# Performance work log

Measured on AMD Instinct MI355X. Metric: run time of the kernel, lower is better.

The kernel has to match this reference:

```python
import jax, jax.numpy as jnp
import numpy as np

B, T = 64, 256
CHAR_V, CHAR_D = 8000, 128
WORD_V, WORD_D = 100000, 300
POS_V, POS_D = 30, 64
SPO_D = 20
D = CHAR_D + WORD_D + POS_D + SPO_D  # 512
L, H, KD, VD, INNER = 4, 8, 64, 64, 2048
C = 25  # num tag classes


def _layer_norm(x, g, b, eps=1e-5):
    m = jnp.mean(x, axis=-1, keepdims=True)
    v = jnp.mean(jnp.square(x - m), axis=-1, keepdims=True)
    return (x - m) * jax.lax.rsqrt(v + eps) * g + b


def setup_inputs() -> dict:
    key = jax.random.key(0)
    ks = jax.random.split(key, 40)
    s = 0.05
    n = lambda k, shp, sc=0.05: jax.random.normal(k, shp, jnp.float32) * sc
    return {
        "char": jax.random.randint(ks[0], (B, T), 0, CHAR_V),
        "word": jax.random.randint(ks[1], (B, T), 0, WORD_V),
        "pos": jax.random.randint(ks[2], (B, T), 0, POS_V),
        "spo": jax.random.normal(ks[3], (B, SPO_D), jnp.float32),
        "seq_len": jax.random.randint(ks[4], (B,), 1, T + 1),
        "tag": jax.random.randint(ks[5], (B, T), 0, C),
        "char_table": n(ks[6], (CHAR_V, CHAR_D)),
        "word_table": n(ks[7], (WORD_V, WORD_D)),
        "pos_table": n(ks[8], (POS_V, POS_D)),
        "ln0_g": jnp.ones((D,), jnp.float32),
        "ln0_b": jnp.zeros((D,), jnp.float32),
        "Wq": n(ks[9], (L, D, H * KD)), "bq": jnp.zeros((L, H * KD), jnp.float32),
        "Wk": n(ks[10], (L, D, H * KD)), "bk": jnp.zeros((L, H * KD), jnp.float32),
        "Wv": n(ks[11], (L, D, H * VD)), "bv": jnp.zeros((L, H * VD), jnp.float32),
        "Wo": n(ks[12], (L, H * VD, D)), "bo": jnp.zeros((L, D), jnp.float32),
        "ln1_g": jnp.ones((L, D), jnp.float32), "ln1_b": jnp.zeros((L, D), jnp.float32),
        "W1": n(ks[13], (L, D, INNER)), "b1": jnp.zeros((L, INNER), jnp.float32),
        "W2": n(ks[14], (L, INNER, D)), "b2": jnp.zeros((L, D), jnp.float32),
        "ln2_g": jnp.ones((L, D), jnp.float32), "ln2_b": jnp.zeros((L, D), jnp.float32),
        "Wout": n(ks[15], (D, C)), "bout": jnp.zeros((C,), jnp.float32),
        "trans": n(ks[16], (C, C)),
    }


def _forward(spo, char_table, word_table, pos_table, ln0_g, ln0_b,
             Wq, bq, Wk, bk, Wv, bv, Wo, bo, ln1_g, ln1_b,
             W1, b1, W2, b2, ln2_g, ln2_b, Wout, bout, trans,
             char, word, pos, seq_len, tag):
    # mask[b,t] = t < seq_len[b]
    mask = (jnp.arange(T)[None, :] < seq_len[:, None]).astype(jnp.float32)  # [B,T]

    # embed + concat + layernorm (dropout in eval mode = identity)
    x = jnp.concatenate([
        char_table[char], word_table[word], pos_table[pos],
        jnp.broadcast_to(spo[:, None, :], (B, T, SPO_D)),
    ], axis=-1)  # [B,T,D]
    x = _layer_norm(x, ln0_g, ln0_b)

    neg_inf = jnp.finfo(x.dtype).min
    key_ok = mask[:, None, None, :] > 0  # [B,1,1,T] key padding mask
    scale = jnp.sqrt(jnp.asarray(KD, x.dtype))
    for l in range(L):
        q = (x @ Wq[l] + bq[l]).reshape(B, T, H, KD).transpose(0, 2, 1, 3)
        k = (x @ Wk[l] + bk[l]).reshape(B, T, H, KD).transpose(0, 2, 1, 3)
        v = (x @ Wv[l] + bv[l]).reshape(B, T, H, VD).transpose(0, 2, 1, 3)
        scores = jnp.einsum('bhqd,bhkd->bhqk', q, k) / scale
        scores = jnp.where(key_ok, scores, neg_inf)
        attn = jax.nn.softmax(scores, axis=-1)
        ctx = jnp.einsum('bhqk,bhkd->bhqd', attn, v).transpose(0, 2, 1, 3).reshape(B, T, H * VD)
        att_out = ctx @ Wo[l] + bo[l]
        h1 = _layer_norm(att_out + x, ln1_g[l], ln1_b[l])
        ff = jax.nn.relu(h1 @ W1[l] + b1[l]) @ W2[l] + b2[l]
        x = _layer_norm(ff + h1, ln2_g[l], ln2_b[l]) * mask[:, :, None]

    logits = x @ Wout + bout  # [B,T,C]

    # ---- CRF negative log likelihood (include_start_end_trans=False) ----
    lg = logits.transpose(1, 0, 2)  # [T,B,C]
    m = mask.T                      # [T,B]

    def step(alpha, inp):
        emit, mt = inp  # emit [B,C], mt [B]
        tmp = alpha[:, :, None] + trans[None, :, :] + emit[:, None, :]  # [B,C,C]
        new = jax.nn.logsumexp(tmp, axis=1)
        alpha = jnp.where(mt[:, None] > 0, new, alpha)
        return alpha, None

    alpha, _ = jax.lax.scan(step, lg[0], (lg[1:], m[1:]))
    log_z = jax.nn.logsumexp(alpha, axis=-1)  # [B]

    tags_t = tag.T  # [T,B]
    emit_gold = jnp.take_along_axis(lg, tags_t[:, :, None], axis=-1)[..., 0] * m  # [T,B]
    trans_gold = trans[tags_t[:-1], tags_t[1:]] * m[1:]  # [T-1,B]
    gold = emit_gold.sum(0) + trans_gold.sum(0)  # [B]

    return jnp.mean(log_z - gold)


def reference(char, word, pos, spo, seq_len, tag, char_table, word_table, pos_table,
              ln0_g, ln0_b, Wq, bq, Wk, bk, Wv, bv, Wo, bo, ln1_g, ln1_b,
              W1, b1, W2, b2, ln2_g, ln2_b, Wout, bout, trans):
    return _forward(spo, char_table, word_table, pos_table, ln0_g, ln0_b,
                    Wq, bq, Wk, bk, Wv, bv, Wo, bo, ln1_g, ln1_b,
                    W1, b1, W2, b2, ln2_g, ln2_b, Wout, bout, trans,
                    char, word, pos, seq_len, tag)
```

## Files before the change

kernel.cpp:

```cpp
#include <hip/hip_runtime.h>
#include <cmath>

namespace {

constexpr int LT = 4;
constexpr int BB = 64;
constexpr int TT = 256;
constexpr int DD = 512;
constexpr int HH = 8;
constexpr int DH = 64;
constexpr int FF = 2048;
constexpr int CC = 25;
constexpr int M_ALL = BB * TT;
constexpr size_t MB = 1024 * 1024;

typedef __attribute__((ext_vector_type(8))) short short8;
typedef __attribute__((ext_vector_type(4))) short short4_;
typedef __attribute__((ext_vector_type(4))) float f32x4;
typedef __attribute__((ext_vector_type(4))) _Float16 half4;

__device__ __forceinline__ float b2f(unsigned short u) {
  union { unsigned int i; float f; } x; x.i = ((unsigned int)u) << 16; return x.f;
}
__device__ __forceinline__ unsigned short f2b(float f) {
  union { float f; unsigned int i; } x; x.f = f;
  unsigned int r = x.i + 0x7FFFu + ((x.i >> 16) & 1u);
  return (unsigned short)(r >> 16);
}
__device__ __forceinline__ float rdlane(float v, int l) {
  union { float f; unsigned int i; } x; x.f = v;
  x.i = (unsigned int)__builtin_amdgcn_readlane((int)x.i, l);
  return x.f;
}
__device__ __forceinline__ void gl_lds16(const void* g, void* l) {
  __builtin_amdgcn_global_load_lds(
      (const __attribute__((address_space(1))) unsigned int*)g,
      (__attribute__((address_space(3))) unsigned int*)l, 16, 0, 0);
}
__device__ __forceinline__ float wredsum(float v) {
#pragma unroll
  for (int o = 32; o > 0; o >>= 1) v += __shfl_xor(v, o, 64);
  return v;
}

__global__ __launch_bounds__(64) void prefix_k(const int* __restrict__ sl,
                                               int* __restrict__ boff) {
  const int l = threadIdx.x;
  int s = sl[l];
#pragma unroll
  for (int o = 1; o < 64; o <<= 1) {
    const int u = __shfl_up(s, o, 64);
    if (l >= o) s += u;
  }
  boff[l + 1] = s;
  if (l == 0) boff[0] = 0;
}

__global__ __launch_bounds__(256) void rowmap_k(const int* __restrict__ sl,
                                                const int* __restrict__ boff,
                                                int* __restrict__ rowmap) {
  const int b = blockIdx.x, t = threadIdx.x;
  if (t < sl[b]) rowmap[boff[b] + t] = (b << 8) | t;
}

template <int NSRC>
__global__ __launch_bounds__(256) void wconv_k(const float* __restrict__ in0,
                                               const float* __restrict__ in1,
                                               const float* __restrict__ in2,
                                               unsigned short* __restrict__ out,
                                               int K, int N, size_t lstride,
                                               size_t sstride) {
  __shared__ float ts[64][65];
  const int k0 = blockIdx.x * 64, n0 = blockIdx.y * 64;
  const float* in = in0;
  if constexpr (NSRC == 3) {
    const int s = blockIdx.z / LT;
    in = (s == 0) ? in0 : (s == 1 ? in1 : in2);
    in += (size_t)(blockIdx.z % LT) * K * N;
    out += (size_t)(blockIdx.z % LT) * lstride + (size_t)(blockIdx.z / LT) * sstride;
  } else {
    in += (size_t)blockIdx.z * K * N;
    out += (size_t)blockIdx.z * lstride;
  }
  const int tid = threadIdx.x;
  for (int i = tid; i < 1024; i += 256) {
    const int r = i >> 4, c4 = i & 15;
    const float4 f = *(const float4*)&in[(size_t)(k0 + r) * N + n0 + c4 * 4];
    ts[r][c4 * 4 + 0] = f.x; ts[r][c4 * 4 + 1] = f.y;
    ts[r][c4 * 4 + 2] = f.z; ts[r][c4 * 4 + 3] = f.w;
  }
  __syncthreads();
  const int n_r = tid >> 2, kc = (tid & 3) * 16;
  short8 v0, v1;
#pragma unroll
  for (int j = 0; j < 8; ++j) {
    v0[j] = (short)f2b(ts[kc + j][n_r]);
    v1[j] = (short)f2b(ts[kc + 8 + j][n_r]);
  }
  unsigned short* op = out + (size_t)(n0 + n_r) * K + k0 + kc;
  *(short8*)op = v0;
  *(short8*)(op + 8) = v1;
}

__global__ __launch_bounds__(256) void embed_ln0_k(
    const int* __restrict__ ch, const int* __restrict__ wd, const int* __restrict__ ps,
    const float* __restrict__ spo, const float* __restrict__ ctab,
    const float* __restrict__ wtab, const float* __restrict__ ptab,
    const float* __restrict__ g, const float* __restrict__ be,
    const int* __restrict__ sl, const int* __restrict__ boff,
    unsigned short* __restrict__ xc) {
  const int row = blockIdx.x * 4 + (threadIdx.x >> 6);
  const int b = row >> 8, t = row & 255;
  if (t >= sl[b]) return;
  const int orow = boff[b] + t;
  const int lane = threadIdx.x & 63;
  const int ci = ch[row], wi = wd[row], pi = ps[row];
  float v[8];
#pragma unroll
  for (int j = 0; j < 2; ++j) {
    const int d = j * 256 + lane * 4;
    float4 f;
    if (d < 128)      f = *(const float4*)&ctab[(size_t)ci * 128 + d];
    else if (d < 428) f = *(const float4*)&wtab[(size_t)wi * 300 + (d - 128)];
    else if (d < 492) f = *(const float4*)&ptab[(size_t)pi * 64 + (d - 428)];
    else              f = *(const float4*)&spo[(size_t)b * 20 + (d - 492)];
    v[j * 4 + 0] = f.x; v[j * 4 + 1] = f.y; v[j * 4 + 2] = f.z; v[j * 4 + 3] = f.w;
  }
  float s = 0.f;
#pragma unroll
  for (int i = 0; i < 8; ++i) s += v[i];
  const float mean = wredsum(s) * (1.0f / 512.0f);
  float vs = 0.f;
#pragma unroll
  for (int i = 0; i < 8; ++i) { const float d = v[i] - mean; vs += d * d; }
  const float rstd = rsqrtf(wredsum(vs) * (1.0f / 512.0f) + 1e-5f);
#pragma unroll
  for (int j = 0; j < 2; ++j) {
    const int d = j * 256 + lane * 4;
    const float4 gv = *(const float4*)&g[d];
    const float4 bv = *(const float4*)&be[d];
    short4_ ob;
    ob[0] = (short)f2b((v[j * 4 + 0] - mean) * rstd * gv.x + bv.x);
    ob[1] = (short)f2b((v[j * 4 + 1] - mean) * rstd * gv.y + bv.y);
    ob[2] = (short)f2b((v[j * 4 + 2] - mean) * rstd * gv.z + bv.z);
    ob[3] = (short)f2b((v[j * 4 + 3] - mean) * rstd * gv.w + bv.w);
    *(short4_*)&xc[(size_t)orow * DD + d] = ob;
  }
}

template <int EPI, int TM>
__global__ __launch_bounds__(256) void gemm_mfma(
    const unsigned short* __restrict__ A, const unsigned short* __restrict__ Bt,
    const float* __restrict__ bias, const float* __restrict__ bias2,
    const float* __restrict__ bias3, const unsigned short* __restrict__ res,
    const int* __restrict__ Mptr, const int* __restrict__ rowmap,
    void* __restrict__ outv, void* __restrict__ out2v, void* __restrict__ out3v,
    int M, int N, int K) {
  constexpr int MI = TM / 32;
  const int Mp = Mptr[0];
  const int m0 = blockIdx.y * TM, n0 = blockIdx.x * 128;
  if (m0 >= Mp) return;
  __shared__ unsigned short As[TM * 64];
  __shared__ unsigned short Bs[128 * 64];
  const int tid = threadIdx.x;
  const int wid = tid >> 6, lane = tid & 63;
  const int wr = wid >> 1, wc = wid & 1;
  const int cl = lane & 15, rg = lane >> 4;
  f32x4 acc[MI][4];
#pragma unroll
  for (int i = 0; i < MI; ++i)
#pragma unroll
    for (int j = 0; j < 4; ++j) acc[i][j] = (f32x4){0.f, 0.f, 0.f, 0.f};

  const int rbase = tid >> 3, sl = tid & 7;
  const int sc = 8 * (sl ^ (rbase & 7));

  for (int k0 = 0; k0 < K; k0 += 64) {
    if (k0) __syncthreads();
#pragma unroll
    for (int i = 0; i < TM / 32; ++i) {
      const int r = i * 32 + rbase;
      gl_lds16(A + (size_t)(m0 + r) * K + k0 + sc, (char*)As + (i * 256 + tid) * 16);
    }
#pragma unroll
    for (int i = 0; i < 4; ++i) {
      const int r = i * 32 + rbase;
      gl_lds16(Bt + (size_t)(n0 + r) * K + k0 + sc, (char*)Bs + (i * 256 + tid) * 16);
    }
    __syncthreads();
#pragma unroll
    for (int ks = 0; ks < 2; ++ks) {
      short8 a[MI], b[4];
      const int kbyte = ks * 64 + rg * 16;
#pragma unroll
      for (int f = 0; f < MI; ++f) {
        const int am = wr * (TM / 2) + f * 16 + cl;
        a[f] = *(const short8*)((const char*)As + am * 128 + (kbyte ^ ((am & 7) << 4)));
      }
#pragma unroll
      for (int f = 0; f < 4; ++f) {
        const int bn = wc * 64 + f * 16 + cl;
        b[f] = *(const short8*)((const char*)Bs + bn * 128 + (kbyte ^ ((bn & 7) << 4)));
      }
#pragma unroll
      for (int mi = 0; mi < MI; ++mi)
#pragma unroll
        for (int ni = 0; ni < 4; ++ni)
          acc[mi][ni] = __builtin_amdgcn_mfma_f32_16x16x32_bf16(a[mi], b[ni],
                                                                acc[mi][ni], 0, 0, 0);
    }
  }

  int rm[MI][4];
  if constexpr (EPI == 5) {
#pragma unroll
    for (int mi = 0; mi < MI; ++mi) {
      const int mb_ = m0 + wr * (TM / 2) + mi * 16 + rg * 4;
#pragma unroll
      for (int i = 0; i < 4; ++i)
        rm[mi][i] = (mb_ + i < Mp) ? rowmap[mb_ + i] : -1;
    }
  }

#pragma unroll
  for (int ni = 0; ni < 4; ++ni) {
    const int n = n0 + wc * 64 + ni * 16 + cl;
    float bv;
    if constexpr (EPI == 5) {
      bv = (n < 512) ? bias[n] : (n < 1024 ? bias2[n - 512] : bias3[n - 1024]);
    } else {
      bv = bias[n];
    }
#pragma unroll
    for (int mi = 0; mi < MI; ++mi) {
      if constexpr (EPI == 5) {
        const int hh = (n >> 6) & 7, d = n & 63;
        if (n < 1024) {
          unsigned short* outp = (unsigned short*)((n < 512) ? outv : out2v);
#pragma unroll
          for (int i = 0; i < 4; ++i) {
            const int rmv = rm[mi][i];
            if (rmv >= 0) {
              const int bb = rmv >> 8, tt = rmv & 255;
              outp[(((size_t)(bb * HH + hh) * TT + tt) << 6) + d] =
                  f2b(acc[mi][ni][i] + bv);
            }
          }
        } else {
          const int rm0 = rm[mi][0];
          if (rm0 >= 0 && rm[mi][3] == rm0 + 3) {
            half4 pk;
#pragma unroll
            for (int i = 0; i < 4; ++i) pk[i] = (_Float16)(acc[mi][ni][i] + bv);
            *(half4*)((_Float16*)out3v +
                      ((((size_t)((rm0 >> 8) * HH + hh) * DH + d) << 8) + (rm0 & 255))) = pk;
          } else {
#pragma unroll
            for (int i = 0; i < 4; ++i) {
              const int rmv = rm[mi][i];
              if (rmv >= 0)
                ((_Float16*)out3v)[(((size_t)((rmv >> 8) * HH + hh) * DH + d) << 8) +
                                   (rmv & 255)] = (_Float16)(acc[mi][ni][i] + bv);
            }
          }
        }
      } else {
#pragma unroll
        for (int i = 0; i < 4; ++i) {
          const int m = m0 + wr * (TM / 2) + mi * 16 + rg * 4 + i;
          const float v = acc[mi][ni][i] + bv;
          if constexpr (EPI == 1) {
            ((unsigned short*)outv)[(size_t)m * N + n] = f2b(fmaxf(v, 0.f));
          } else if constexpr (EPI == 7) {
            ((unsigned short*)outv)[(size_t)m * N + n] =
                f2b(v + b2f(res[(size_t)m * N + n]));
          }
        }
      }
    }
  }
}

__global__ __launch_bounds__(256) void attn_mfma_k(
    const unsigned short* __restrict__ qb, const unsigned short* __restrict__ kbp,
    const _Float16* __restrict__ vtp, const int* __restrict__ seq_len,
    const int* __restrict__ boff, unsigned short* __restrict__ cb) {
  __shared__ unsigned short Ks[256 * 64];
  __shared__ _Float16 Vs[64 * 256];
  __shared__ unsigned short Os[64 * 64];
  const int bh = blockIdx.x;
  const int b = bh >> 3, h = bh & 7;
  const int tid = threadIdx.x;
  const int wid = tid >> 6, lane = tid & 63;
  const int cl = lane & 15, rg = lane >> 4;
  const int len = seq_len[b];
  const int off = boff[b];

  {
    const int r = tid >> 3, sl = tid & 7;
#pragma unroll
    for (int i = 0; i < 8; ++i) {
      if (i * 32 < len) {
        const int row = i * 32 + r;
        gl_lds16(kbp + ((size_t)bh * TT + row) * DH + 8 * (sl ^ (row & 7)),
                 (char*)Ks + (i * 256 + tid) * 16);
      }
    }
#pragma unroll
    for (int i = 0; i < 8; ++i) {
      const int u = i * 256 + tid;
      const int vrow = u >> 5, vsl = u & 31;
      gl_lds16(vtp + ((size_t)bh * DH + vrow) * TT + 8 * (vsl ^ (vrow & 7)),
               (char*)Vs + u * 16);
    }
  }
  __syncthreads();

  for (int qt4 = 0; qt4 < 4; ++qt4) {
    if (qt4 * 64 >= len) break;
    f32x4 o[4];
#pragma unroll
    for (int db = 0; db < 4; ++db) o[db] = (f32x4){0.f, 0.f, 0.f, 0.f};
    {
      const int q0 = qt4 * 64 + wid * 16;
      short8 bqf[2];
      const unsigned short* qp = qb + ((size_t)bh * TT + q0 + cl) * DH + rg * 8;
      bqf[0] = *(const short8*)qp;
      bqf[1] = *(const short8*)(qp + 32);
      f32x4 s[16];
#pragma unroll
      for (int kk = 0; kk < 16; ++kk) {
        s[kk] = (f32x4){0.f, 0.f, 0.f, 0.f};
        if (kk * 16 < len) {
          const int row = kk * 16 + cl;
          const char* base = (const char*)Ks + row * 128;
          const int sw = (row & 7) << 4;
          const short8 a0 = *(const short8*)(base + ((rg * 16) ^ sw));
          const short8 a1 = *(const short8*)(base + ((64 + rg * 16) ^ sw));
          s[kk] = __builtin_amdgcn_mfma_f32_16x16x32_bf16(a0, bqf[0], s[kk], 0, 0, 0);
          s[kk] = __builtin_amdgcn_mfma_f32_16x16x32_bf16(a1, bqf[1], s[kk], 0, 0, 0);
        }
      }
      float mx = -3.0e38f;
#pragma unroll
      for (int kk = 0; kk < 16; ++kk)
        if (kk * 16 < len) {
#pragma unroll
          for (int i = 0; i < 4; ++i) {
            float v = s[kk][i] * 0.125f;
            v = (kk * 16 + rg * 4 + i < len) ? v : -3.0e38f;
            s[kk][i] = v;
            mx = fmaxf(mx, v);
          }
        }
      mx = fmaxf(mx, __shfl_xor(mx, 16, 64));
      mx = fmaxf(mx, __shfl_xor(mx, 32, 64));
      float lsum = 0.f;
#pragma unroll
      for (int kk = 0; kk < 16; ++kk)
        if (kk * 16 < len) {
#pragma unroll
          for (int i = 0; i < 4; ++i) {
            const float p = __expf(s[kk][i] - mx);
            s[kk][i] = p;
            lsum += p;
          }
        }
      lsum += __shfl_xor(lsum, 16, 64);
      lsum += __shfl_xor(lsum, 32, 64);
      const float rl = 1.0f / lsum;
#pragma unroll
      for (int kk = 0; kk < 16; ++kk)
        if (kk * 16 < len) {
          half4 bp;
#pragma unroll
          for (int i = 0; i < 4; ++i) bp[i] = (_Float16)(s[kk][i] * rl);
#pragma unroll
          for (int db = 0; db < 4; ++db) {
            const int vrow = db * 16 + cl;
            const int byte = kk * 32 + rg * 8;
            const half4 a = *(const half4*)((const char*)Vs + vrow * 512 +
                              ((byte & ~15) ^ ((vrow & 7) << 4)) + (byte & 15));
            o[db] = __builtin_amdgcn_mfma_f32_16x16x16f16(a, bp, o[db], 0, 0, 0);
          }
        }
    }
    __syncthreads();
    {
      const int orow = wid * 16 + cl;
      char* obase = (char*)Os + orow * 128;
      const int sw = (orow & 7) << 4;
#pragma unroll
      for (int db = 0; db < 4; ++db) {
        short4_ pk;
#pragma unroll
        for (int i = 0; i < 4; ++i) pk[i] = (short)f2b(o[db][i]);
        const int byte = db * 32 + rg * 8;
        *(short4_*)(obase + ((byte & ~15) ^ sw) + (byte & 15)) = pk;
      }
    }
    __syncthreads();
    {
      const int r = tid >> 2, part = tid & 3;
      const int t = qt4 * 64 + r;
      if (t < len) {
        const int sw = (r & 7) << 4;
        const char* rbase = (const char*)Os + r * 128;
        const short8 w0 = *(const short8*)(rbase + ((part * 32) ^ sw));
        const short8 w1 = *(const short8*)(rbase + ((part * 32 + 16) ^ sw));
        unsigned short* dst = cb + ((size_t)(off + t)) * DD + h * DH + part * 16;
        *(short8*)dst = w0;
        *(short8*)(dst + 8) = w1;
      }
    }
  }
}

__global__ __launch_bounds__(256) void ln_k(const unsigned short* __restrict__ a,
                                            const float* __restrict__ g,
                                            const float* __restrict__ be,
                                            const int* __restrict__ Mptr,
                                            unsigned short* __restrict__ outb) {
  const int row = blockIdx.x * 4 + (threadIdx.x >> 6);
  if (row >= Mptr[0]) return;
  const int lane = threadIdx.x & 63;
  float v[8];
  {
    const short8 va = *(const short8*)&a[(size_t)row * DD + lane * 8];
#pragma unroll
    for (int i = 0; i < 8; ++i) v[i] = b2f((unsigned short)va[i]);
  }
  float s = 0.f;
#pragma unroll
  for (int i = 0; i < 8; ++i) s += v[i];
  const float mean = wredsum(s) * (1.0f / 512.0f);
  float vs = 0.f;
#pragma unroll
  for (int i = 0; i < 8; ++i) { const float d = v[i] - mean; vs += d * d; }
  const float rstd = rsqrtf(wredsum(vs) * (1.0f / 512.0f) + 1e-5f);
  const float4 g0 = *(const float4*)&g[lane * 8];
  const float4 g1 = *(const float4*)&g[lane * 8 + 4];
  const float4 b0 = *(const float4*)&be[lane * 8];
  const float4 b1 = *(const float4*)&be[lane * 8 + 4];
  const float gg[8] = {g0.x, g0.y, g0.z, g0.w, g1.x, g1.y, g1.z, g1.w};
  const float bb[8] = {b0.x, b0.y, b0.z, b0.w, b1.x, b1.y, b1.z, b1.w};
  short8 ob;
#pragma unroll
  for (int i = 0; i < 8; ++i)
    ob[i] = (short)f2b((v[i] - mean) * rstd * gg[i] + bb[i]);
  *(short8*)&outb[(size_t)row * DD + lane * 8] = ob;
}

__global__ __launch_bounds__(256) void logits_k(const unsigned short* __restrict__ xb,
                                                const float* __restrict__ W,
                                                const float* __restrict__ bo,
                                                const int* __restrict__ Mptr,
                                                float* __restrict__ lg) {
  const int r0 = blockIdx.x * 8;
  if (r0 >= Mptr[0]) return;
  __shared__ float xs[8][516];
  for (int i = threadIdx.x; i < 512; i += 256) {
    const int rr = i >> 6, c8 = (i & 63) * 8;
    const short8 v = *(const short8*)&xb[(size_t)(r0 + rr) * DD + c8];
#pragma unroll
    for (int j = 0; j < 8; ++j) xs[rr][c8 + j] = b2f((unsigned short)v[j]);
  }
  __syncthreads();
  const int r = threadIdx.x >> 5, c = threadIdx.x & 31;
  if (c < CC) {
    float acc = 0.f;
#pragma unroll 8
    for (int k = 0; k < DD; ++k) acc += xs[r][k] * W[k * CC + c];
    lg[(size_t)(r0 + r) * CC + c] = acc + bo[c];
  }
}

__global__ __launch_bounds__(64) void crf_k(const float* __restrict__ lg,
                                            const int* __restrict__ tag,
                                            const int* __restrict__ seq_len,
                                            const int* __restrict__ boff,
                                            const float* __restrict__ trans,
                                            float* __restrict__ nll) {
  __shared__ float eexp[TT * CC + 64];
  __shared__ float tr[CC * CC];
  const int b = blockIdx.x;
  const int l = threadIdx.x;
  const int len = seq_len[b];
  const float* lgb = lg + (size_t)boff[b] * CC;
  for (int i = l; i < len * CC; i += 64) eexp[i] = __expf(lgb[i]);
  for (int i = l; i < CC * CC; i += 64) tr[i] = trans[i];
  __syncthreads();
  const int lc = (l < CC) ? l : (CC - 1);
  float et[CC];
#pragma unroll
  for (int i = 0; i < CC; ++i) et[i] = __expf(tr[i * CC + lc]);
  const float e00 = lgb[0];
  float M = e00;
  float A = (l < CC) ? __expf(lgb[l] - e00) : 0.f;
  for (int t = 1; t < len; ++t) {
    const float e = eexp[t * CC + lc];
    float s0 = 0.f, s1 = 0.f, s2 = 0.f, s3 = 0.f, s4 = 0.f;
#pragma unroll
    for (int i = 0; i < CC; i += 5) {
      s0 += rdlane(A, i + 0) * et[i + 0];
      s1 += rdlane(A, i + 1) * et[i + 1];
      s2 += rdlane(A, i + 2) * et[i + 2];
      s3 += rdlane(A, i + 3) * et[i + 3];
      s4 += rdlane(A, i + 4) * et[i + 4];
    }
    A = (((s0 + s1) + (s2 + s3)) + s4) * e;
    if ((t & 3) == 0) {
      const float r = rdlane(A, 0);
      M += __logf(r);
      A *= __builtin_amdgcn_rcpf(r);
    }
  }
  const float tot = wredsum((l < CC) ? A : 0.f);
  float gold = 0.f;
  for (int t = l; t < len; t += 64)
    gold += lgb[t * CC + tag[b * TT + t]];
  for (int t = 1 + l; t < len; t += 64)
    gold += tr[tag[b * TT + t - 1] * CC + tag[b * TT + t]];
  gold = wredsum(gold);
  if (l == 0) nll[b] = (M + __logf(tot)) - gold;
}

__global__ __launch_bounds__(64) void final_k(const float* __restrict__ nll,
                                              float* __restrict__ out) {
  float v = nll[threadIdx.x];
  v = wredsum(v);
  if (threadIdx.x == 0) out[0] = v * (1.0f / 64.0f);
}

}

extern "C" void kernel_launch(void* const* d_in, const int* in_sizes, int n_in,
                              void* d_out, int out_size, void* d_ws, size_t ws_size,
                              hipStream_t stream) {
  (void)in_sizes; (void)n_in; (void)out_size; (void)ws_size;
  const int* chi = (const int*)d_in[0];
  const int* wdi = (const int*)d_in[1];
  const int* psi = (const int*)d_in[2];
  const float* spo = (const float*)d_in[3];
  const int* seq_len = (const int*)d_in[4];
  const int* tag = (const int*)d_in[5];
  const float* ctab = (const float*)d_in[6];
  const float* wtab = (const float*)d_in[7];
  const float* ptab = (const float*)d_in[8];
  const float* ln0g = (const float*)d_in[9];
  const float* ln0b = (const float*)d_in[10];
  const float* Wq = (const float*)d_in[11];
  const float* bq = (const float*)d_in[12];
  const float* Wk = (const float*)d_in[13];
  const float* bk = (const float*)d_in[14];
  const float* Wv = (const float*)d_in[15];
  const float* bv = (const float*)d_in[16];
  const float* Wo = (const float*)d_in[17];
  const float* bo = (const float*)d_in[18];
  const float* ln1g = (const float*)d_in[19];
  const float* ln1b = (const float*)d_in[20];
  const float* W1 = (const float*)d_in[21];
  const float* b1 = (const float*)d_in[22];
  const float* W2 = (const float*)d_in[23];
  const float* b2 = (const float*)d_in[24];
  const float* ln2g = (const float*)d_in[25];
  const float* ln2b = (const float*)d_in[26];
  const float* Wout = (const float*)d_in[27];
  const float* bout = (const float*)d_in[28];
  const float* trans = (const float*)d_in[29];

  char* w8 = (char*)d_ws;
  unsigned short* ib  = (unsigned short*)(w8);
  unsigned short* xc  = (unsigned short*)(w8 + 64 * MB);
  unsigned short* cbx = (unsigned short*)(w8 + 80 * MB);
  unsigned short* ab  = (unsigned short*)(w8 + 96 * MB);
  unsigned short* hb  = (unsigned short*)(w8 + 112 * MB);
  unsigned short* t0b = (unsigned short*)(w8 + 128 * MB);
  unsigned short* qbuf = (unsigned short*)(w8 + 144 * MB);
  unsigned short* kbuf = (unsigned short*)(w8 + 160 * MB);
  _Float16* vtb = (_Float16*)(w8 + 176 * MB);
  unsigned short* wqkv = (unsigned short*)(w8 + 192 * MB);
  unsigned short* wot = (unsigned short*)(w8 + 198 * MB);
  unsigned short* w1t = (unsigned short*)(w8 + 200 * MB);
  unsigned short* w2t = (unsigned short*)(w8 + 208 * MB);
  float* lg = (float*)(w8 + 216 * MB);
  float* nll = (float*)(w8 + 218 * MB);
  int* boff = (int*)(w8 + 219 * MB);
  int* rowmap = (int*)(w8 + 220 * MB);
  const int* Mptr = boff + 64;

  prefix_k<<<1, 64, 0, stream>>>(seq_len, boff);
  rowmap_k<<<BB, 256, 0, stream>>>(seq_len, boff, rowmap);

  const size_t QKVS = (size_t)1536 * 512;
  wconv_k<3><<<dim3(8, 8, 3 * LT), 256, 0, stream>>>(
      Wq, Wk, Wv, wqkv, DD, DD, QKVS, (size_t)512 * 512);
  wconv_k<1><<<dim3(8, 8, LT), 256, 0, stream>>>(
      Wo, nullptr, nullptr, wot, DD, DD, (size_t)DD * DD, 0);
  wconv_k<1><<<dim3(8, 32, LT), 256, 0, stream>>>(
      W1, nullptr, nullptr, w1t, DD, FF, (size_t)DD * FF, 0);
  wconv_k<1><<<dim3(32, 8, LT), 256, 0, stream>>>(
      W2, nullptr, nullptr, w2t, FF, DD, (size_t)FF * DD, 0);

  embed_ln0_k<<<M_ALL / 4, 256, 0, stream>>>(chi, wdi, psi, spo, ctab, wtab, ptab,
                                             ln0g, ln0b, seq_len, boff, xc);

  for (int l = 0; l < LT; ++l) {
    gemm_mfma<5, 64><<<dim3(12, M_ALL / 64), 256, 0, stream>>>(
        xc, wqkv + (size_t)l * QKVS, bq + l * DD, bk + l * DD, bv + l * DD,
        nullptr, Mptr, rowmap, qbuf, kbuf, vtb, M_ALL, 1536, DD);
    attn_mfma_k<<<BB * HH, 256, 0, stream>>>(qbuf, kbuf, vtb, seq_len, boff, cbx);
    gemm_mfma<7, 64><<<dim3(4, M_ALL / 64), 256, 0, stream>>>(
        cbx, wot + (size_t)l * DD * DD, bo + l * DD, nullptr, nullptr,
        xc, Mptr, nullptr, ab, nullptr, nullptr, M_ALL, DD, DD);
    ln_k<<<M_ALL / 4, 256, 0, stream>>>(ab, ln1g + l * DD, ln1b + l * DD, Mptr, hb);
    gemm_mfma<1, 64><<<dim3(FF / 128, M_ALL / 64), 256, 0, stream>>>(
        hb, w1t + (size_t)l * FF * DD, b1 + l * FF, nullptr, nullptr,
        nullptr, Mptr, nullptr, ib, nullptr, nullptr, M_ALL, FF, DD);
    gemm_mfma<7, 64><<<dim3(DD / 128, M_ALL / 64), 256, 0, stream>>>(
        ib, w2t + (size_t)l * FF * DD, b2 + l * DD, nullptr, nullptr,
        hb, Mptr, nullptr, t0b, nullptr, nullptr, M_ALL, DD, FF);
    ln_k<<<M_ALL / 4, 256, 0, stream>>>(t0b, ln2g + l * DD, ln2b + l * DD, Mptr, xc);
  }
  logits_k<<<M_ALL / 8, 256, 0, stream>>>(xc, Wout, bout, Mptr, lg);
  crf_k<<<BB, 64, 0, stream>>>(lg, tag, seq_len, boff, trans, nll);
  final_k<<<1, 64, 0, stream>>>(nll, (float*)d_out);
}
```

Before: 842.8 us.

## Triple-buffer LDS tiles in MFMA GEMM with async global-to-LDS prefetch

Replaces the single-buffer load-sync-compute loop in the bf16 MFMA GEMM with a 3-stage LDS ring. Tiles for k+2 are issued via direct global-to-LDS loads while the current tile is computed, and partial vmcnt waits let only the oldest stage be awaited. The goal is to hide global memory latency behind MFMA work. In exchange, LDS use triples, which may reduce occupancy, and correctness depends on the vmcnt count matching the number of loads per stage.

```diff
diff --git a/kernel.cpp b/kernel.cpp
--- a/kernel.cpp
+++ b/kernel.cpp
@@ -157,11 +157,13 @@
     void* __restrict__ outv, void* __restrict__ out2v, void* __restrict__ out3v,
     int M, int N, int K) {
   constexpr int MI = TM / 32;
+  constexpr int ND = 3;
+  constexpr int LPT = TM / 32 + 4;
   const int Mp = Mptr[0];
   const int m0 = blockIdx.y * TM, n0 = blockIdx.x * 128;
   if (m0 >= Mp) return;
-  __shared__ unsigned short As[TM * 64];
-  __shared__ unsigned short Bs[128 * 64];
+  __shared__ unsigned short As[ND][TM * 64];
+  __shared__ unsigned short Bs[ND][128 * 64];
   const int tid = threadIdx.x;
   const int wid = tid >> 6, lane = tid & 63;
   const int wr = wid >> 1, wc = wid & 1;
@@ -175,19 +177,34 @@
   const int rbase = tid >> 3, sl = tid & 7;
   const int sc = 8 * (sl ^ (rbase & 7));
 
-  for (int k0 = 0; k0 < K; k0 += 64) {
-    if (k0) __syncthreads();
+  auto stage = [&](int buf, int k0) {
 #pragma unroll
     for (int i = 0; i < TM / 32; ++i) {
       const int r = i * 32 + rbase;
-      gl_lds16(A + (size_t)(m0 + r) * K + k0 + sc, (char*)As + (i * 256 + tid) * 16);
+      gl_lds16(A + (size_t)(m0 + r) * K + k0 + sc,
+               (char*)As[buf] + (i * 256 + tid) * 16);
     }
 #pragma unroll
     for (int i = 0; i < 4; ++i) {
       const int r = i * 32 + rbase;
-      gl_lds16(Bt + (size_t)(n0 + r) * K + k0 + sc, (char*)Bs + (i * 256 + tid) * 16);
-    }
-    __syncthreads();
+      gl_lds16(Bt + (size_t)(n0 + r) * K + k0 + sc,
+               (char*)Bs[buf] + (i * 256 + tid) * 16);
+    }
+  };
+
+  const int NT = K >> 6;
+  stage(0, 0);
+  stage(1, 64);
+  int cur = 0;
+  for (int t = 0; t < NT; ++t) {
+    if (t < NT - 1)
+      asm volatile("s_waitcnt vmcnt(%0)" :: "i"(LPT) : "memory");
+    else
+      asm volatile("s_waitcnt vmcnt(0)" ::: "memory");
+    __builtin_amdgcn_s_barrier();
+    if (t + ND - 1 < NT) stage((t + ND - 1) % ND, (t + ND - 1) << 6);
+    const char* Ab = (const char*)As[cur];
+    const char* Bb = (const char*)Bs[cur];
 #pragma unroll
     for (int ks = 0; ks < 2; ++ks) {
       short8 a[MI], b[4];
@@ -195,12 +212,12 @@
 #pragma unroll
       for (int f = 0; f < MI; ++f) {
         const int am = wr * (TM / 2) + f * 16 + cl;
-        a[f] = *(const short8*)((const char*)As + am * 128 + (kbyte ^ ((am & 7) << 4)));
+        a[f] = *(const short8*)(Ab + am * 128 + (kbyte ^ ((am & 7) << 4)));
       }
 #pragma unroll
       for (int f = 0; f < 4; ++f) {
         const int bn = wc * 64 + f * 16 + cl;
-        b[f] = *(const short8*)((const char*)Bs + bn * 128 + (kbyte ^ ((bn & 7) << 4)));
+        b[f] = *(const short8*)(Bb + bn * 128 + (kbyte ^ ((bn & 7) << 4)));
       }
 #pragma unroll
       for (int mi = 0; mi < MI; ++mi)
@@ -209,6 +226,7 @@
           acc[mi][ni] = __builtin_amdgcn_mfma_f32_16x16x32_bf16(a[mi], b[ni],
                                                                 acc[mi][ni], 0, 0, 0);
     }
+    cur = (cur + 1 == ND) ? 0 : cur + 1;
   }
 
   int rm[MI][4];
```

Result: slower. 960.1 us (+13.9%).
